# Optimization experiments

Measured on AMD Instinct MI355X. Metric: run time of the kernel, lower is better.

The kernel has to match this reference:

```python
import jax, jax.numpy as jnp
import numpy as np

B, C, H, W = 16, 256, 56, 56
WH, WW = 7, 7
NH = 8            # heads
HID = 1024        # mlp hidden = int(4*dim)
N = WH * WW
EPS = 1e-5


def _rel_index():
    # mirrors the torch buffer computation in Rel_Attention.__init__
    coords = np.stack(np.meshgrid(np.arange(WH), np.arange(WW), indexing='ij')).reshape(2, -1)  # (2, N)
    rel = coords[:, :, None] - coords[:, None, :]  # (2, N, N)
    rel[0] += WH - 1
    rel[1] += WW - 1
    rel[0] *= 2 * WW - 1
    return jnp.asarray(rel.sum(0).reshape(-1))  # (N*N,)

REL_IDX = _rel_index()


def channel_ln(x, w, b):
    # LayerNorm over channel dim of NCHW tensor (permute -> LN -> permute back)
    xt = x.transpose(0, 2, 3, 1)  # BHWC
    mu = xt.mean(-1, keepdims=True)
    var = xt.var(-1, keepdims=True)
    xt = (xt - mu) / jnp.sqrt(var + EPS) * w + b
    return xt.transpose(0, 3, 1, 2)


def to_blocks(x):
    # (B,C,H,W) -> (B, H/wh, W/ww, C, wh, ww)
    b, c, h, w = x.shape
    x = x.reshape(b, c, h // WH, WH, w // WW, WW)
    return x.transpose(0, 2, 4, 1, 3, 5)


def unblock(x):
    # faithful to original: reshape(B, C, Hb*win_W, Hb*win_W)  (square sizes)
    b, hb, wb, c, wh, ww = x.shape
    return x.transpose(0, 3, 1, 4, 2, 5).reshape(b, c, hb * ww, hb * ww)


def rel_attention(xw, qkv_w, qkv_b, proj_w, proj_b, table):
    b, hb, wb, c = xw.shape[:4]
    hd = c // NH
    scale = hd ** (-0.5)
    xf = xw.reshape(-1, c, N)                                  # (M, C, N)
    qkv = jnp.einsum('oc,mcn->mon', qkv_w, xf) + qkv_b[None, :, None]
    q, k, v = jnp.split(qkv, 3, axis=1)

    def heads(t):
        return t.reshape(-1, NH, hd, N).transpose(0, 1, 3, 2)  # (M, h, N, d)

    q, k, v = heads(q), heads(k), heads(v)
    bias = table[REL_IDX].reshape(N, N, NH).transpose(2, 0, 1)  # (h, N, N)
    attn = jnp.einsum('mhnd,mhkd->mhnk', q, k) * scale + bias
    attn = jax.nn.softmax(attn, axis=-1)
    o = jnp.einsum('mhnk,mhkd->mhnd', attn, v)                 # (M, h, N, d)
    o = o.transpose(0, 1, 3, 2).reshape(-1, c, N)              # (M, C, N)
    o = jnp.einsum('oc,mcn->mon', proj_w, o) + proj_b[None, :, None]
    return o.reshape(b, hb, wb, c, WH, WW)


def mlp(x, fc1_w, fc1_b, fc2_w, fc2_b):
    h = jnp.einsum('oc,bchw->bohw', fc1_w, x) + fc1_b[None, :, None, None]
    h = jax.nn.gelu(h, approximate=False)
    return jnp.einsum('oc,bchw->bohw', fc2_w, h) + fc2_b[None, :, None, None]


def setup_inputs() -> dict:
    key = jax.random.key(0)
    ks = jax.random.split(key, 8)
    s = 0.02
    return {
        'x': jax.random.normal(ks[0], (B, C, H, W), jnp.float32),
        'ln1_w': jnp.ones((C,), jnp.float32),
        'ln1_b': jnp.zeros((C,), jnp.float32),
        'ln2_w': jnp.ones((C,), jnp.float32),
        'ln2_b': jnp.zeros((C,), jnp.float32),
        'qkv_w': jax.random.normal(ks[1], (3 * C, C), jnp.float32) * s,
        'qkv_b': jnp.zeros((3 * C,), jnp.float32),
        'proj_w': jax.random.normal(ks[2], (C, C), jnp.float32) * s,
        'proj_b': jnp.zeros((C,), jnp.float32),
        'rel_bias_table': jax.random.normal(ks[3], ((2 * WH - 1) * (2 * WW - 1), NH), jnp.float32) * s,
        'fc1_w': jax.random.normal(ks[4], (HID, C), jnp.float32) * s,
        'fc1_b': jnp.zeros((HID,), jnp.float32),
        'fc2_w': jax.random.normal(ks[5], (C, HID), jnp.float32) * s,
        'fc2_b': jnp.zeros((C,), jnp.float32),
    }


def reference(x, ln1_w, ln1_b, ln2_w, ln2_b, qkv_w, qkv_b, proj_w, proj_b,
              rel_bias_table, fc1_w, fc1_b, fc2_w, fc2_b):
    out = to_blocks(channel_ln(x, ln1_w, ln1_b))
    out = rel_attention(out, qkv_w, qkv_b, proj_w, proj_b, rel_bias_table)
    # original applies attn a second time before unblocking
    out = rel_attention(out, qkv_w, qkv_b, proj_w, proj_b, rel_bias_table)
    x = x + unblock(out)
    x = x + mlp(channel_ln(x, ln2_w, ln2_b), fc1_w, fc1_b, fc2_w, fc2_b)
    return x
```

## Files before the change

kernel.cpp:

```cpp
#include <hip/hip_runtime.h>
#include <stdint.h>

typedef uint16_t u16;
typedef short bf16x8 __attribute__((ext_vector_type(8)));
typedef float f32x4 __attribute__((ext_vector_type(4)));

__device__ __forceinline__ float bf2f(u16 s) {
  union { unsigned int i; float f; } c; c.i = ((unsigned int)s) << 16; return c.f;
}
__device__ __forceinline__ u16 f2bf(float f) {
  union { float f; unsigned int i; } c; c.f = f;
  unsigned int u = c.i;
  u += 0x7FFFu + ((u >> 16) & 1u);
  return (u16)(u >> 16);
}
__device__ __forceinline__ f32x4 mfma16(bf16x8 a, bf16x8 b, f32x4 c) {
  return __builtin_amdgcn_mfma_f32_16x16x32_bf16(a, b, c, 0, 0, 0);
}
__device__ __forceinline__ int dtype_flag(const u16* ln1w_raw) { return ln1w_raw[0] == 0x3F80 ? 1 : 0; }
__device__ __forceinline__ float loadF(const void* p, size_t i, int flag) {
  return flag ? bf2f(((const u16*)p)[i]) : ((const float*)p)[i];
}

#define OFF_QKVW 0
#define OFF_QKVB 196608
#define OFF_PROJW 197376
#define OFF_PROJB 262912
#define OFF_REL 263168
#define OFF_FC1W 264520
#define OFF_FC1B 526664
#define OFF_FC2W 527688
#define OFF_FC2B 789832
#define OFF_LN1W 790088
#define OFF_LN1B 790344
#define OFF_LN2W 790600
#define OFF_LN2B 790856
#define WC_TOTAL 791112

__global__ __launch_bounds__(256) void k_convert(const u16* __restrict__ ln1w_raw,
    const void* qkvw, const void* qkvb, const void* projw, const void* projb,
    const void* rel, const void* fc1w, const void* fc1b, const void* fc2w, const void* fc2b,
    const void* ln1w, const void* ln1b, const void* ln2w, const void* ln2b,
    u16* __restrict__ dst) {
  const int flag = dtype_flag(ln1w_raw);
  int i = blockIdx.x * 256 + threadIdx.x;
  if (i >= WC_TOTAL) return;
  const void* src; int off;
  if      (i < OFF_QKVB)  { src = qkvw;  off = i - OFF_QKVW; }
  else if (i < OFF_PROJW) { src = qkvb;  off = i - OFF_QKVB; }
  else if (i < OFF_PROJB) { src = projw; off = i - OFF_PROJW; }
  else if (i < OFF_REL)   { src = projb; off = i - OFF_PROJB; }
  else if (i < OFF_FC1W)  { src = rel;   off = i - OFF_REL; }
  else if (i < OFF_FC1B)  { src = fc1w;  off = i - OFF_FC1W; }
  else if (i < OFF_FC2W)  { src = fc1b;  off = i - OFF_FC1B; }
  else if (i < OFF_FC2B)  { src = fc2w;  off = i - OFF_FC2W; }
  else if (i < OFF_LN1W)  { src = fc2b;  off = i - OFF_FC2B; }
  else if (i < OFF_LN1B)  { src = ln1w;  off = i - OFF_LN1W; }
  else if (i < OFF_LN2W)  { src = ln1b;  off = i - OFF_LN1B; }
  else if (i < OFF_LN2B)  { src = ln2w;  off = i - OFF_LN2W; }
  else                    { src = ln2b;  off = i - OFF_LN2B; }
  if (i < OFF_QKVB) {
    int j = off & 7, li = (off >> 3) & 63, c0i = (off >> 9) & 7, grp = off >> 12;
    off = (grp * 16 + (li & 15)) * 256 + c0i * 32 + (li >> 4) * 8 + j;
  } else if (i >= OFF_PROJW && i < OFF_PROJB) {
    int j = off & 7, li = (off >> 3) & 63, c0i = (off >> 9) & 7, grp = off >> 12;
    off = (grp * 16 + (li & 15)) * 256 + c0i * 32 + (li >> 4) * 8 + j;
  } else if (i >= OFF_FC1W && i < OFF_FC1B) {
    int j = off & 7, li = (off >> 3) & 63, hj = (off >> 9) & 1, c0i = (off >> 10) & 7,
        w = (off >> 13) & 3, ch = off >> 15;
    off = (ch * 128 + w * 32 + hj * 16 + (li & 15)) * 256 + c0i * 32 + (li >> 4) * 8 + j;
  } else if (i >= OFF_FC2W && i < OFF_FC2B) {
    int j = off & 7, li = (off >> 3) & 63, oct = (off >> 9) & 3, kki = (off >> 11) & 3,
        ch = (off >> 13) & 7, w = off >> 16;
    off = (w * 64 + oct * 16 + (li & 15)) * 1024 + ch * 128 + kki * 32 + (li >> 4) * 8 + j;
  }
  dst[i] = flag ? ((const u16*)src)[off] : f2bf(((const float*)src)[off]);
}

__global__ __launch_bounds__(256) void k_ln1b(const void* __restrict__ xin,
                                              const u16* __restrict__ ln1w_raw,
                                              const u16* __restrict__ lw,
                                              const u16* __restrict__ lb,
                                              u16* __restrict__ win) {
  const int flag = dtype_flag(ln1w_raw);
  __shared__ float tile[56 * 257];
  __shared__ float smu[56], srs[56];
  const int bid = blockIdx.x;
  const int b = bid / 56, h = bid - b * 56;
  const int t = threadIdx.x;
  const int hb = h / 7, ph = h - hb * 7;
  {
    const int lane = t & 63, wq = t >> 6;
    if (lane < 56) {
#pragma unroll 4
      for (int ci = 0; ci < 64; ++ci) {
        const int c = ci * 4 + wq;
        const size_t addr = ((size_t)(b * 256 + c) * 56 + h) * 56 + lane;
        tile[lane * 257 + c] = loadF(xin, addr, flag);
      }
    }
  }
  __syncthreads();
  {
    const int row = t >> 2, qq = t & 3;
    float s = 0.f, q = 0.f;
    if (row < 56) {
      const float* tr = &tile[row * 257 + qq];
#pragma unroll 8
      for (int c0 = 0; c0 < 64; ++c0) { float v = tr[c0 * 4]; s += v; q += v * v; }
    }
    s += __shfl_xor(s, 1, 64); q += __shfl_xor(q, 1, 64);
    s += __shfl_xor(s, 2, 64); q += __shfl_xor(q, 2, 64);
    if (row < 56 && qq == 0) {
      float mm = s * (1.f / 256.f);
      float var = q * (1.f / 256.f) - mm * mm;
      smu[row] = mm; srs[row] = rsqrtf(var + 1e-5f);
    }
  }
  __syncthreads();
#pragma unroll
  for (int i = 0; i < 7; ++i) {
    int eid8 = i * 256 + t;
    int wp = eid8 >> 5, c8 = (eid8 & 31) << 3;
    const float mm = smu[wp], rs = srs[wp];
    const int m = b * 64 + hb * 8 + (wp / 7), n = ph * 7 + (wp % 7);
    bf16x8 o;
#pragma unroll
    for (int j = 0; j < 8; ++j) {
      int c = c8 + j;
      o[j] = (short)f2bf((tile[wp * 257 + c] - mm) * rs * bf2f(lw[c]) + bf2f(lb[c]));
    }
    *(bf16x8*)&win[(size_t)m * 12544 + n * 256 + c8] = o;
  }
}

__global__ __launch_bounds__(512) void k_attn_stage(const u16* __restrict__ win,
                                                    const u16* __restrict__ qkvw,
                                                    const u16* __restrict__ qkvb,
                                                    const u16* __restrict__ rel,
                                                    const u16* __restrict__ projw,
                                                    const u16* __restrict__ projb,
                                                    u16* __restrict__ wout) {
  __shared__ __align__(16) u16 xs[64 * 264];
  __shared__ __align__(16) u16 wa[8][7424];
  const int m = blockIdx.x;
  const int t = threadIdx.x;
  const int w = t >> 6, li = t & 63, lane = li & 15, quad = li >> 4;
  const int hg = w;
  const f32x4 z = {0.f, 0.f, 0.f, 0.f};
  const u16* src = win + (size_t)m * 12544;
#pragma unroll
  for (int i = 0; i < 4; ++i) {
    int chunk = i * 512 + t;
    if (chunk < 1568) {
      int n = chunk >> 5, cc = (chunk & 31) << 3;
      *(bf16x8*)&xs[n * 264 + cc] = *(const bf16x8*)&src[chunk << 3];
    }
  }
  for (int i = t; i < 15 * 264; i += 512) xs[49 * 264 + i] = 0;
  u16* qw = wa[w];
  u16* kw = wa[w] + 2560;
  u16* vw = wa[w] + 5120;
  u16* Pw = wa[w];
  u16* Os = xs;
  for (int i = li; i < 15 * 40; i += 64) { qw[49 * 40 + i] = 0; kw[49 * 40 + i] = 0; }
  for (int i = li; i < 32 * 15; i += 64) { int d = i / 15, j = i - d * 15; vw[d * 72 + 49 + j] = 0; }
  __syncthreads();
  const float SCALE = 0.17677669529663687f;
#pragma unroll
  for (int part = 0; part < 2; ++part) {
    const int obase = part * 256 + hg * 32;
    f32x4 acc[4][2];
#pragma unroll
    for (int i = 0; i < 4; ++i) { acc[i][0] = z; acc[i][1] = z; }
#pragma unroll
    for (int c0i = 0; c0i < 8; ++c0i) {
      bf16x8 a[4], b[2];
#pragma unroll
      for (int nt = 0; nt < 4; ++nt)
        a[nt] = *(const bf16x8*)&xs[(nt * 16 + lane) * 264 + c0i * 32 + quad * 8];
#pragma unroll
      for (int oj = 0; oj < 2; ++oj)
        b[oj] = *(const bf16x8*)&qkvw[(size_t)(((part * 16 + hg * 2 + oj) * 8 + c0i) * 64 + li) * 8];
#pragma unroll
      for (int nt = 0; nt < 4; ++nt)
#pragma unroll
        for (int oj = 0; oj < 2; ++oj) acc[nt][oj] = mfma16(a[nt], b[oj], acc[nt][oj]);
    }
    u16* dstL = part ? kw : qw;
#pragma unroll
    for (int oj = 0; oj < 2; ++oj) {
      const int d = oj * 16 + lane;
      const float bias = bf2f(qkvb[obase + d]);
#pragma unroll
      for (int nt = 0; nt < 4; ++nt)
#pragma unroll
        for (int r = 0; r < 4; ++r) {
          int n = nt * 16 + quad * 4 + r;
          if (n < 49) dstL[n * 40 + d] = f2bf(acc[nt][oj][r] + bias);
        }
    }
  }
  {
    f32x4 acc[2][4];
#pragma unroll
    for (int i = 0; i < 2; ++i)
#pragma unroll
      for (int j = 0; j < 4; ++j) acc[i][j] = z;
#pragma unroll
    for (int c0i = 0; c0i < 8; ++c0i) {
      bf16x8 a[2], b[4];
#pragma unroll
      for (int vj = 0; vj < 2; ++vj)
        a[vj] = *(const bf16x8*)&qkvw[(size_t)(((32 + hg * 2 + vj) * 8 + c0i) * 64 + li) * 8];
#pragma unroll
      for (int nt = 0; nt < 4; ++nt)
        b[nt] = *(const bf16x8*)&xs[(nt * 16 + lane) * 264 + c0i * 32 + quad * 8];
#pragma unroll
      for (int vj = 0; vj < 2; ++vj)
#pragma unroll
        for (int nt = 0; nt < 4; ++nt) acc[vj][nt] = mfma16(a[vj], b[nt], acc[vj][nt]);
    }
#pragma unroll
    for (int vj = 0; vj < 2; ++vj)
#pragma unroll
      for (int r = 0; r < 4; ++r) {
        const int d = vj * 16 + quad * 4 + r;
        const float bias = bf2f(qkvb[512 + hg * 32 + d]);
#pragma unroll
        for (int nt = 0; nt < 4; ++nt) {
          int n = nt * 16 + lane;
          if (n < 49) vw[d * 72 + n] = f2bf(acc[vj][nt][r] + bias);
        }
      }
  }
  __syncthreads();
  f32x4 s[4][4];
  {
    bf16x8 aq[4], bk[4];
#pragma unroll
    for (int nt = 0; nt < 4; ++nt) {
      aq[nt] = *(const bf16x8*)&qw[(nt * 16 + lane) * 40 + quad * 8];
      bk[nt] = *(const bf16x8*)&kw[(nt * 16 + lane) * 40 + quad * 8];
    }
#pragma unroll
    for (int i = 0; i < 4; ++i)
#pragma unroll
      for (int j = 0; j < 4; ++j) s[i][j] = mfma16(aq[i], bk[j], z);
  }
#pragma unroll
  for (int nt1 = 0; nt1 < 4; ++nt1) {
#pragma unroll
    for (int r = 0; r < 4; ++r) {
      int n1 = nt1 * 16 + quad * 4 + r;
      int n1c = n1 < 49 ? n1 : 48;
      int ph1 = n1c / 7, pw1 = n1c - ph1 * 7;
      float v[4];
#pragma unroll
      for (int j = 0; j < 4; ++j) {
        int n2 = j * 16 + lane;
        if (n2 < 49) {
          int ph2 = n2 / 7, pw2 = n2 - ph2 * 7;
          int idx = (ph1 - ph2 + 6) * 13 + (pw1 - pw2 + 6);
          v[j] = s[nt1][j][r] * SCALE + bf2f(rel[idx * 8 + hg]);
        } else v[j] = -1e30f;
      }
      float mx = fmaxf(fmaxf(v[0], v[1]), fmaxf(v[2], v[3]));
      for (int off = 1; off < 16; off <<= 1) mx = fmaxf(mx, __shfl_xor(mx, off, 64));
      float e0 = __expf(v[0] - mx), e1 = __expf(v[1] - mx);
      float e2 = __expf(v[2] - mx), e3 = __expf(v[3] - mx);
      float sum = e0 + e1 + e2 + e3;
      for (int off = 1; off < 16; off <<= 1) sum += __shfl_xor(sum, off, 64);
      float rinv = __builtin_amdgcn_rcpf(sum);
      Pw[n1 * 72 + 0 * 16 + lane] = f2bf(e0 * rinv);
      Pw[n1 * 72 + 1 * 16 + lane] = f2bf(e1 * rinv);
      Pw[n1 * 72 + 2 * 16 + lane] = f2bf(e2 * rinv);
      Pw[n1 * 72 + 3 * 16 + lane] = f2bf(e3 * rinv);
    }
  }
  {
    f32x4 o[4][2];
#pragma unroll
    for (int i = 0; i < 4; ++i) { o[i][0] = z; o[i][1] = z; }
#pragma unroll
    for (int kc = 0; kc < 2; ++kc) {
      bf16x8 ap[4], bv[2];
#pragma unroll
      for (int nt1 = 0; nt1 < 4; ++nt1)
        ap[nt1] = *(const bf16x8*)&Pw[(nt1 * 16 + lane) * 72 + kc * 32 + quad * 8];
#pragma unroll
      for (int dt = 0; dt < 2; ++dt)
        bv[dt] = *(const bf16x8*)&vw[(dt * 16 + lane) * 72 + kc * 32 + quad * 8];
#pragma unroll
      for (int nt1 = 0; nt1 < 4; ++nt1)
#pragma unroll
        for (int dt = 0; dt < 2; ++dt) o[nt1][dt] = mfma16(ap[nt1], bv[dt], o[nt1][dt]);
    }
#pragma unroll
    for (int nt1 = 0; nt1 < 4; ++nt1)
#pragma unroll
      for (int dt = 0; dt < 2; ++dt)
#pragma unroll
        for (int r = 0; r < 4; ++r) {
          int n1 = nt1 * 16 + quad * 4 + r;
          if (n1 < 49) Os[n1 * 264 + hg * 32 + dt * 16 + lane] = f2bf(o[nt1][dt][r]);
        }
  }
  __syncthreads();
  {
    f32x4 acc[4][2];
#pragma unroll
    for (int i = 0; i < 4; ++i) { acc[i][0] = z; acc[i][1] = z; }
#pragma unroll
    for (int c0i = 0; c0i < 8; ++c0i) {
      bf16x8 a[4], b[2];
#pragma unroll
      for (int nt = 0; nt < 4; ++nt)
        a[nt] = *(const bf16x8*)&Os[(nt * 16 + lane) * 264 + c0i * 32 + quad * 8];
#pragma unroll
      for (int oj = 0; oj < 2; ++oj)
        b[oj] = *(const bf16x8*)&projw[(size_t)(((w * 2 + oj) * 8 + c0i) * 64 + li) * 8];
#pragma unroll
      for (int nt = 0; nt < 4; ++nt)
#pragma unroll
        for (int oj = 0; oj < 2; ++oj) acc[nt][oj] = mfma16(a[nt], b[oj], acc[nt][oj]);
    }
#pragma unroll
    for (int oj = 0; oj < 2; ++oj) {
      const int oc = w * 32 + oj * 16 + lane;
      const float bias = bf2f(projb[oc]);
#pragma unroll
      for (int nt = 0; nt < 4; ++nt)
#pragma unroll
        for (int r = 0; r < 4; ++r) {
          int n = nt * 16 + quad * 4 + r;
          if (n < 49) wout[(size_t)m * 12544 + n * 256 + oc] = f2bf(acc[nt][oj][r] + bias);
        }
    }
  }
}

__global__ __launch_bounds__(256) void k_resid2(const void* __restrict__ xin,
                                                const u16* __restrict__ ln1w_raw,
                                                const u16* __restrict__ attn,
                                                const u16* __restrict__ l2w,
                                                const u16* __restrict__ l2b,
                                                u16* __restrict__ xrn,
                                                u16* __restrict__ ln2d) {
  const int flag = dtype_flag(ln1w_raw);
  __shared__ float tile[56 * 257];
  __shared__ float smu[56], srs[56];
  const int bid = blockIdx.x;
  const int b = bid / 56, h = bid - b * 56;
  const int t = threadIdx.x;
  const int hb = h / 7, ph = h - hb * 7;
#pragma unroll
  for (int i = 0; i < 7; ++i) {
    int eid8 = i * 256 + t;
    int wp = eid8 >> 5, c8 = (eid8 & 31) << 3;
    int mm = b * 64 + hb * 8 + (wp / 7), nn = ph * 7 + (wp % 7);
    bf16x8 v = *(const bf16x8*)&attn[(size_t)mm * 12544 + nn * 256 + c8];
    float* dst = &tile[wp * 257 + c8];
#pragma unroll
    for (int j = 0; j < 8; ++j) dst[j] = bf2f((u16)v[j]);
  }
  __syncthreads();
  {
    const int lane = t & 63, wq = t >> 6;
    if (lane < 56) {
#pragma unroll 4
      for (int ci = 0; ci < 64; ++ci) {
        const int c = ci * 4 + wq;
        const size_t addr = ((size_t)(b * 256 + c) * 56 + h) * 56 + lane;
        float v = tile[lane * 257 + c] + loadF(xin, addr, flag);
        tile[lane * 257 + c] = v;
        xrn[addr] = f2bf(v);
      }
    }
  }
  __syncthreads();
  {
    const int row = t >> 2, qq = t & 3;
    float s = 0.f, q = 0.f;
    if (row < 56) {
      const float* tr = &tile[row * 257 + qq];
#pragma unroll 8
      for (int c0 = 0; c0 < 64; ++c0) { float v = tr[c0 * 4]; s += v; q += v * v; }
    }
    s += __shfl_xor(s, 1, 64); q += __shfl_xor(q, 1, 64);
    s += __shfl_xor(s, 2, 64); q += __shfl_xor(q, 2, 64);
    if (row < 56 && qq == 0) {
      float mm = s * (1.f / 256.f);
      float var = q * (1.f / 256.f) - mm * mm;
      smu[row] = mm; srs[row] = rsqrtf(var + 1e-5f);
    }
  }
  __syncthreads();
#pragma unroll
  for (int i = 0; i < 7; ++i) {
    int eid8 = i * 256 + t;
    int wp = eid8 >> 5, c8 = (eid8 & 31) << 3;
    const float mm = smu[wp], rs = srs[wp];
    bf16x8 o;
#pragma unroll
    for (int j = 0; j < 8; ++j) {
      int c = c8 + j;
      o[j] = (short)f2bf((tile[wp * 257 + c] - mm) * rs * bf2f(l2w[c]) + bf2f(l2b[c]));
    }
    const int p = b * 3136 + h * 56 + wp;
    const int pblk = p >> 6, pt = (p & 63) >> 4, r16 = p & 15;
    const int c0i = c8 >> 5, quad = (c8 >> 3) & 3;
    *(bf16x8*)&ln2d[(size_t)((((pblk * 4 + pt) * 8 + c0i) * 64 + quad * 16 + r16)) << 3] = o;
  }
}

__global__ __launch_bounds__(256, 3) void k_mlp2(const u16* __restrict__ aG,
                                                 const u16* __restrict__ w1,
                                                 const u16* __restrict__ b1,
                                                 const u16* __restrict__ w2,
                                                 const u16* __restrict__ b2,
                                                 const u16* __restrict__ xrn,
                                                 const u16* __restrict__ ln1w_raw,
                                                 void* __restrict__ out) {
  const int flag = dtype_flag(ln1w_raw);
  __shared__ __align__(16) u16 arena[25088];
  u16* xp = arena;
  u16* g  = arena + 16384;
  const int pblk = blockIdx.x;
  const int pix0 = pblk * 64;
  const int t = threadIdx.x;
  const int w = t >> 6, li = t & 63, lane = li & 15, quad = li >> 4;
  {
    const u16* asrc = aG + (size_t)pblk * 16384;
#pragma unroll
    for (int i = 0; i < 8; ++i) {
      int idx = i * 256 + t;
      *(bf16x8*)&xp[idx * 8] = *(const bf16x8*)&asrc[(size_t)idx * 8];
    }
  }
  __syncthreads();
  const f32x4 z = {0.f, 0.f, 0.f, 0.f};
  f32x4 acc2[4][4];
#pragma unroll
  for (int i = 0; i < 4; ++i)
#pragma unroll
    for (int j = 0; j < 4; ++j) acc2[i][j] = z;

  auto fc1 = [&](int ch) {
    f32x4 a1[4][2];
#pragma unroll
    for (int i = 0; i < 4; ++i) { a1[i][0] = z; a1[i][1] = z; }
#pragma unroll
    for (int c0i = 0; c0i < 8; ++c0i) {
      bf16x8 av[4], bw[2];
#pragma unroll
      for (int pt = 0; pt < 4; ++pt)
        av[pt] = *(const bf16x8*)&xp[((pt * 8 + c0i) * 64 + li) * 8];
#pragma unroll
      for (int hj = 0; hj < 2; ++hj)
        bw[hj] = *(const bf16x8*)&w1[(size_t)((((ch * 4 + w) * 8 + c0i) * 2 + hj) * 64 + li) * 8];
#pragma unroll
      for (int pt = 0; pt < 4; ++pt)
#pragma unroll
        for (int hj = 0; hj < 2; ++hj) a1[pt][hj] = mfma16(av[pt], bw[hj], a1[pt][hj]);
    }
#pragma unroll
    for (int hj = 0; hj < 2; ++hj) {
      const int hl = w * 32 + hj * 16 + lane;
      const float bias = bf2f(b1[ch * 128 + hl]);
#pragma unroll
      for (int pt = 0; pt < 4; ++pt)
#pragma unroll
        for (int r = 0; r < 4; ++r) {
          float u_ = a1[pt][hj][r] + bias;
          float y = u_ * fmaf(u_ * u_, 0.035677408136300125f, 0.7978845608028654f);
          float e2 = __expf(-2.f * y);
          float v = u_ * __builtin_amdgcn_rcpf(1.f + e2);
          g[(pt * 16 + quad * 4 + r) * 136 + hl] = f2bf(v);
        }
    }
  };
  auto fc2 = [&](int ch) {
#pragma unroll
    for (int kki = 0; kki < 4; ++kki) {
      bf16x8 aw[4], bg[4];
#pragma unroll
      for (int oct = 0; oct < 4; ++oct)
        aw[oct] = *(const bf16x8*)&w2[(size_t)((((w * 8 + ch) * 4 + kki) * 4 + oct) * 64 + li) * 8];
#pragma unroll
      for (int pt = 0; pt < 4; ++pt)
        bg[pt] = *(const bf16x8*)&g[(pt * 16 + lane) * 136 + kki * 32 + quad * 8];
#pragma unroll
      for (int oct = 0; oct < 4; ++oct)
#pragma unroll
        for (int pt = 0; pt < 4; ++pt) acc2[oct][pt] = mfma16(aw[oct], bg[pt], acc2[oct][pt]);
    }
  };

  fc1(0);
  __syncthreads();
#pragma unroll 1
  for (int ch = 0; ch < 8; ++ch) {
    fc2(ch);
    if (ch < 7) {
      __syncthreads();
      fc1(ch + 1);
      __syncthreads();
    }
  }

  float* Ob = (float*)arena;
  const int b_ = pix0 / 3136, rem0 = pix0 - b_ * 3136;
  const int sub = t & 7, r0 = t >> 3;
#pragma unroll 1
  for (int e = 0; e < 2; ++e) {
    __syncthreads();
    if ((w >> 1) == e) {
      const int wl = w & 1;
#pragma unroll
      for (int oct = 0; oct < 4; ++oct)
#pragma unroll
        for (int pt = 0; pt < 4; ++pt)
#pragma unroll
          for (int r = 0; r < 4; ++r)
            Ob[(wl * 64 + oct * 16 + quad * 4 + r) * 65 + pt * 16 + lane] = acc2[oct][pt][r];
    }
    __syncthreads();
    bf16x8 xr[4];
    size_t addrs[4];
#pragma unroll
    for (int i = 0; i < 4; ++i) {
      const int oc = e * 128 + i * 32 + r0;
      addrs[i] = (size_t)(b_ * 256 + oc) * 3136 + rem0 + sub * 8;
      xr[i] = *(const bf16x8*)&xrn[addrs[i]];
    }
#pragma unroll
    for (int i = 0; i < 4; ++i) {
      const int oc = e * 128 + i * 32 + r0;
      const float bias = bf2f(b2[oc]);
      const float* obr = &Ob[(i * 32 + r0) * 65 + sub * 8];
      float v[8];
#pragma unroll
      for (int j = 0; j < 8; ++j)
        v[j] = obr[j] + bias + bf2f((u16)xr[i][j]);
      if (flag) {
        bf16x8 o8;
#pragma unroll
        for (int j = 0; j < 8; ++j) o8[j] = (short)f2bf(v[j]);
        *(bf16x8*)&((u16*)out)[addrs[i]] = o8;
      } else {
        float* dst = &((float*)out)[addrs[i]];
        f32x4 lo = {v[0], v[1], v[2], v[3]}, hi = {v[4], v[5], v[6], v[7]};
        *(f32x4*)&dst[0] = lo;
        *(f32x4*)&dst[4] = hi;
      }
    }
  }
}

extern "C" void kernel_launch(void* const* d_in, const int* in_sizes, int n_in,
                              void* d_out, int out_size, void* d_ws, size_t ws_size,
                              hipStream_t stream) {
  (void)in_sizes; (void)n_in; (void)out_size; (void)ws_size;
  const void* x     = d_in[0];
  const u16* ln1w_raw = (const u16*)d_in[1];
  u16* ws = (u16*)d_ws;
  const size_t R = 12845056;
  u16* R0 = ws;
  u16* R1 = ws + R;
  u16* R2 = ws + 2 * R;
  u16* WC = ws + 3 * R;
  const u16* qkvw_c = WC + OFF_QKVW;
  const u16* qkvb_c = WC + OFF_QKVB;
  const u16* projw_c = WC + OFF_PROJW;
  const u16* projb_c = WC + OFF_PROJB;
  const u16* rel_c  = WC + OFF_REL;
  const u16* fc1w_c = WC + OFF_FC1W;
  const u16* fc1b_c = WC + OFF_FC1B;
  const u16* fc2w_c = WC + OFF_FC2W;
  const u16* fc2b_c = WC + OFF_FC2B;
  const u16* ln1w_c = WC + OFF_LN1W;
  const u16* ln1b_c = WC + OFF_LN1B;
  const u16* ln2w_c = WC + OFF_LN2W;
  const u16* ln2b_c = WC + OFF_LN2B;

  k_convert<<<(WC_TOTAL + 255) / 256, 256, 0, stream>>>(
      ln1w_raw, d_in[5], d_in[6], d_in[7], d_in[8], d_in[9],
      d_in[10], d_in[11], d_in[12], d_in[13], d_in[1], d_in[2], d_in[3], d_in[4], WC);

  k_ln1b      <<<896, 256, 0, stream>>>(x, ln1w_raw, ln1w_c, ln1b_c, R0);
  k_attn_stage<<<1024, 512, 0, stream>>>(R0, qkvw_c, qkvb_c, rel_c, projw_c, projb_c, R1);
  k_attn_stage<<<1024, 512, 0, stream>>>(R1, qkvw_c, qkvb_c, rel_c, projw_c, projb_c, R2);
  k_resid2    <<<896, 256, 0, stream>>>(x, ln1w_raw, R2, ln2w_c, ln2b_c, R0, R1);
  k_mlp2      <<<784, 256, 0, stream>>>(R1, fc1w_c, fc1b_c, fc2w_c, fc2b_c, R0, ln1w_raw, d_out);
}
```

Before: 515.5 us.

## Fuse both attention passes into one kernel and vectorize LN global loads

The two back-to-back attention stage launches become one kernel that loops twice over the same window. The first pass's projection output is written back into the shared-memory input tile instead of global memory, which removes one launch and a full global write and read of the intermediate. The LN1 and residual kernels now load x with 16-byte vector loads along W and store the residual as packed vectors. MFMA sections are wrapped in s_setprio raises. In exchange there are extra barriers and longer-lived blocks, and register pressure may rise.

After: 792.1 us. +53.7%, slower.

```diff
diff --git a/kernel.cpp b/kernel.cpp
--- a/kernel.cpp
+++ b/kernel.cpp
@@ -2,6 +2,7 @@
 #include <stdint.h>
 
 typedef uint16_t u16;
+typedef short bf16x4 __attribute__((ext_vector_type(4)));
 typedef short bf16x8 __attribute__((ext_vector_type(8)));
 typedef float f32x4 __attribute__((ext_vector_type(4)));
 
@@ -89,15 +90,25 @@
   const int b = bid / 56, h = bid - b * 56;
   const int t = threadIdx.x;
   const int hb = h / 7, ph = h - hb * 7;
-  {
-    const int lane = t & 63, wq = t >> 6;
-    if (lane < 56) {
-#pragma unroll 4
-      for (int ci = 0; ci < 64; ++ci) {
-        const int c = ci * 4 + wq;
-        const size_t addr = ((size_t)(b * 256 + c) * 56 + h) * 56 + lane;
-        tile[lane * 257 + c] = loadF(xin, addr, flag);
-      }
+  if (!flag) {
+#pragma unroll
+    for (int i = 0; i < 14; ++i) {
+      int chunk = i * 256 + t;
+      int c = chunk / 14, w4 = (chunk - c * 14) * 4;
+      const float* xp4 = (const float*)xin + ((size_t)(b * 256 + c) * 56 + h) * 56 + w4;
+      f32x4 v = *(const f32x4*)xp4;
+#pragma unroll
+      for (int k = 0; k < 4; ++k) tile[(w4 + k) * 257 + c] = v[k];
+    }
+  } else {
+#pragma unroll
+    for (int i = 0; i < 7; ++i) {
+      int chunk = i * 256 + t;
+      int c = chunk / 7, w8 = (chunk - c * 7) * 8;
+      const u16* xp8 = (const u16*)xin + ((size_t)(b * 256 + c) * 56 + h) * 56 + w8;
+      bf16x8 v = *(const bf16x8*)xp8;
+#pragma unroll
+      for (int k = 0; k < 8; ++k) tile[(w8 + k) * 257 + c] = bf2f((u16)v[k]);
     }
   }
   __syncthreads();
@@ -167,175 +178,205 @@
   for (int i = li; i < 32 * 15; i += 64) { int d = i / 15, j = i - d * 15; vw[d * 72 + 49 + j] = 0; }
   __syncthreads();
   const float SCALE = 0.17677669529663687f;
-#pragma unroll
-  for (int part = 0; part < 2; ++part) {
-    const int obase = part * 256 + hg * 32;
-    f32x4 acc[4][2];
-#pragma unroll
-    for (int i = 0; i < 4; ++i) { acc[i][0] = z; acc[i][1] = z; }
-#pragma unroll
-    for (int c0i = 0; c0i < 8; ++c0i) {
-      bf16x8 a[4], b[2];
-#pragma unroll
-      for (int nt = 0; nt < 4; ++nt)
-        a[nt] = *(const bf16x8*)&xs[(nt * 16 + lane) * 264 + c0i * 32 + quad * 8];
-#pragma unroll
-      for (int oj = 0; oj < 2; ++oj)
-        b[oj] = *(const bf16x8*)&qkvw[(size_t)(((part * 16 + hg * 2 + oj) * 8 + c0i) * 64 + li) * 8];
-#pragma unroll
-      for (int nt = 0; nt < 4; ++nt)
-#pragma unroll
-        for (int oj = 0; oj < 2; ++oj) acc[nt][oj] = mfma16(a[nt], b[oj], acc[nt][oj]);
-    }
-    u16* dstL = part ? kw : qw;
-#pragma unroll
-    for (int oj = 0; oj < 2; ++oj) {
-      const int d = oj * 16 + lane;
-      const float bias = bf2f(qkvb[obase + d]);
-#pragma unroll
-      for (int nt = 0; nt < 4; ++nt)
+#pragma unroll 1
+  for (int s_ = 0; s_ < 2; ++s_) {
+#pragma unroll
+    for (int part = 0; part < 2; ++part) {
+      const int obase = part * 256 + hg * 32;
+      f32x4 acc[4][2];
+#pragma unroll
+      for (int i = 0; i < 4; ++i) { acc[i][0] = z; acc[i][1] = z; }
+#pragma unroll
+      for (int c0i = 0; c0i < 8; ++c0i) {
+        bf16x8 a[4], b[2];
+#pragma unroll
+        for (int nt = 0; nt < 4; ++nt)
+          a[nt] = *(const bf16x8*)&xs[(nt * 16 + lane) * 264 + c0i * 32 + quad * 8];
+#pragma unroll
+        for (int oj = 0; oj < 2; ++oj)
+          b[oj] = *(const bf16x8*)&qkvw[(size_t)(((part * 16 + hg * 2 + oj) * 8 + c0i) * 64 + li) * 8];
+        __builtin_amdgcn_s_setprio(1);
+#pragma unroll
+        for (int nt = 0; nt < 4; ++nt)
+#pragma unroll
+          for (int oj = 0; oj < 2; ++oj) acc[nt][oj] = mfma16(a[nt], b[oj], acc[nt][oj]);
+        __builtin_amdgcn_s_setprio(0);
+      }
+      u16* dstL = part ? kw : qw;
+#pragma unroll
+      for (int oj = 0; oj < 2; ++oj) {
+        const int d = oj * 16 + lane;
+        const float bias = bf2f(qkvb[obase + d]);
+#pragma unroll
+        for (int nt = 0; nt < 4; ++nt)
+#pragma unroll
+          for (int r = 0; r < 4; ++r) {
+            int n = nt * 16 + quad * 4 + r;
+            if (n < 49) dstL[n * 40 + d] = f2bf(acc[nt][oj][r] + bias);
+          }
+      }
+    }
+    {
+      f32x4 acc[2][4];
+#pragma unroll
+      for (int i = 0; i < 2; ++i)
+#pragma unroll
+        for (int j = 0; j < 4; ++j) acc[i][j] = z;
+#pragma unroll
+      for (int c0i = 0; c0i < 8; ++c0i) {
+        bf16x8 a[2], b[4];
+#pragma unroll
+        for (int vj = 0; vj < 2; ++vj)
+          a[vj] = *(const bf16x8*)&qkvw[(size_t)(((32 + hg * 2 + vj) * 8 + c0i) * 64 + li) * 8];
+#pragma unroll
+        for (int nt = 0; nt < 4; ++nt)
+          b[nt] = *(const bf16x8*)&xs[(nt * 16 + lane) * 264 + c0i * 32 + quad * 8];
+        __builtin_amdgcn_s_setprio(1);
+#pragma unroll
+        for (int vj = 0; vj < 2; ++vj)
+#pragma unroll
+          for (int nt = 0; nt < 4; ++nt) acc[vj][nt] = mfma16(a[vj], b[nt], acc[vj][nt]);
+        __builtin_amdgcn_s_setprio(0);
+      }
+#pragma unroll
+      for (int vj = 0; vj < 2; ++vj)
 #pragma unroll
         for (int r = 0; r < 4; ++r) {
-          int n = nt * 16 + quad * 4 + r;
-          if (n < 49) dstL[n * 40 + d] = f2bf(acc[nt][oj][r] + bias);
+          const int d = vj * 16 + quad * 4 + r;
+          const float bias = bf2f(qkvb[512 + hg * 32 + d]);
+#pragma unroll
+          for (int nt = 0; nt < 4; ++nt) {
+            int n = nt * 16 + lane;
+            if (n < 49) vw[d * 72 + n] = f2bf(acc[vj][nt][r] + bias);
+          }
         }
     }
-  }
-  {
-    f32x4 acc[2][4];
-#pragma unroll
-    for (int i = 0; i < 2; ++i)
-#pragma unroll
-      for (int j = 0; j < 4; ++j) acc[i][j] = z;
-#pragma unroll
-    for (int c0i = 0; c0i < 8; ++c0i) {
-      bf16x8 a[2], b[4];
-#pragma unroll
-      for (int vj = 0; vj < 2; ++vj)
-        a[vj] = *(const bf16x8*)&qkvw[(size_t)(((32 + hg * 2 + vj) * 8 + c0i) * 64 + li) * 8];
-#pragma unroll
-      for (int nt = 0; nt < 4; ++nt)
-        b[nt] = *(const bf16x8*)&xs[(nt * 16 + lane) * 264 + c0i * 32 + quad * 8];
-#pragma unroll
-      for (int vj = 0; vj < 2; ++vj)
-#pragma unroll
-        for (int nt = 0; nt < 4; ++nt) acc[vj][nt] = mfma16(a[vj], b[nt], acc[vj][nt]);
-    }
-#pragma unroll
-    for (int vj = 0; vj < 2; ++vj)
+    __syncthreads();
+    f32x4 s[4][4];
+    {
+      bf16x8 aq[4], bk[4];
+#pragma unroll
+      for (int nt = 0; nt < 4; ++nt) {
+        aq[nt] = *(const bf16x8*)&qw[(nt * 16 + lane) * 40 + quad * 8];
+        bk[nt] = *(const bf16x8*)&kw[(nt * 16 + lane) * 40 + quad * 8];
+      }
+      __builtin_amdgcn_s_setprio(1);
+#pragma unroll
+      for (int i = 0; i < 4; ++i)
+#pragma unroll
+        for (int j = 0; j < 4; ++j) s[i][j] = mfma16(aq[i], bk[j], z);
+      __builtin_amdgcn_s_setprio(0);
+    }
+#pragma unroll
+    for (int nt1 = 0; nt1 < 4; ++nt1) {
 #pragma unroll
       for (int r = 0; r < 4; ++r) {
-        const int d = vj * 16 + quad * 4 + r;
-        const float bias = bf2f(qkvb[512 + hg * 32 + d]);
-#pragma unroll
-        for (int nt = 0; nt < 4; ++nt) {
-          int n = nt * 16 + lane;
-          if (n < 49) vw[d * 72 + n] = f2bf(acc[vj][nt][r] + bias);
+        int n1 = nt1 * 16 + quad * 4 + r;
+        int n1c = n1 < 49 ? n1 : 48;
+        int ph1 = n1c / 7, pw1 = n1c - ph1 * 7;
+        float v[4];
+#pragma unroll
+        for (int j = 0; j < 4; ++j) {
+          int n2 = j * 16 + lane;
+          if (n2 < 49) {
+            int ph2 = n2 / 7, pw2 = n2 - ph2 * 7;
+            int idx = (ph1 - ph2 + 6) * 13 + (pw1 - pw2 + 6);
+            v[j] = s[nt1][j][r] * SCALE + bf2f(rel[idx * 8 + hg]);
+          } else v[j] = -1e30f;
         }
-      }
-  }
-  __syncthreads();
-  f32x4 s[4][4];
-  {
-    bf16x8 aq[4], bk[4];
-#pragma unroll
-    for (int nt = 0; nt < 4; ++nt) {
-      aq[nt] = *(const bf16x8*)&qw[(nt * 16 + lane) * 40 + quad * 8];
-      bk[nt] = *(const bf16x8*)&kw[(nt * 16 + lane) * 40 + quad * 8];
-    }
-#pragma unroll
-    for (int i = 0; i < 4; ++i)
-#pragma unroll
-      for (int j = 0; j < 4; ++j) s[i][j] = mfma16(aq[i], bk[j], z);
-  }
-#pragma unroll
-  for (int nt1 = 0; nt1 < 4; ++nt1) {
-#pragma unroll
-    for (int r = 0; r < 4; ++r) {
-      int n1 = nt1 * 16 + quad * 4 + r;
-      int n1c = n1 < 49 ? n1 : 48;
-      int ph1 = n1c / 7, pw1 = n1c - ph1 * 7;
-      float v[4];
-#pragma unroll
-      for (int j = 0; j < 4; ++j) {
-        int n2 = j * 16 + lane;
-        if (n2 < 49) {
-          int ph2 = n2 / 7, pw2 = n2 - ph2 * 7;
-          int idx = (ph1 - ph2 + 6) * 13 + (pw1 - pw2 + 6);
-          v[j] = s[nt1][j][r] * SCALE + bf2f(rel[idx * 8 + hg]);
-        } else v[j] = -1e30f;
-      }
-      float mx = fmaxf(fmaxf(v[0], v[1]), fmaxf(v[2], v[3]));
-      for (int off = 1; off < 16; off <<= 1) mx = fmaxf(mx, __shfl_xor(mx, off, 64));
-      float e0 = __expf(v[0] - mx), e1 = __expf(v[1] - mx);
-      float e2 = __expf(v[2] - mx), e3 = __expf(v[3] - mx);
-      float sum = e0 + e1 + e2 + e3;
-      for (int off = 1; off < 16; off <<= 1) sum += __shfl_xor(sum, off, 64);
-      float rinv = __builtin_amdgcn_rcpf(sum);
-      Pw[n1 * 72 + 0 * 16 + lane] = f2bf(e0 * rinv);
-      Pw[n1 * 72 + 1 * 16 + lane] = f2bf(e1 * rinv);
-      Pw[n1 * 72 + 2 * 16 + lane] = f2bf(e2 * rinv);
-      Pw[n1 * 72 + 3 * 16 + lane] = f2bf(e3 * rinv);
-    }
-  }
-  {
-    f32x4 o[4][2];
-#pragma unroll
-    for (int i = 0; i < 4; ++i) { o[i][0] = z; o[i][1] = z; }
-#pragma unroll
-    for (int kc = 0; kc < 2; ++kc) {
-      bf16x8 ap[4], bv[2];
+        float mx = fmaxf(fmaxf(v[0], v[1]), fmaxf(v[2], v[3]));
+        for (int off = 1; off < 16; off <<= 1) mx = fmaxf(mx, __shfl_xor(mx, off, 64));
+        float e0 = __expf(v[0] - mx), e1 = __expf(v[1] - mx);
+        float e2 = __expf(v[2] - mx), e3 = __expf(v[3] - mx);
+        float sum = e0 + e1 + e2 + e3;
+        for (int off = 1; off < 16; off <<= 1) sum += __shfl_xor(sum, off, 64);
+        float rinv = __builtin_amdgcn_rcpf(sum);
+        Pw[n1 * 72 + 0 * 16 + lane] = f2bf(e0 * rinv);
+        Pw[n1 * 72 + 1 * 16 + lane] = f2bf(e1 * rinv);
+        Pw[n1 * 72 + 2 * 16 + lane] = f2bf(e2 * rinv);
+        Pw[n1 * 72 + 3 * 16 + lane] = f2bf(e3 * rinv);
+      }
+    }
+    {
+      f32x4 o[4][2];
+#pragma unroll
+      for (int i = 0; i < 4; ++i) { o[i][0] = z; o[i][1] = z; }
+#pragma unroll
+      for (int kc = 0; kc < 2; ++kc) {
+        bf16x8 ap[4], bv[2];
+#pragma unroll
+        for (int nt1 = 0; nt1 < 4; ++nt1)
+          ap[nt1] = *(const bf16x8*)&Pw[(nt1 * 16 + lane) * 72 + kc * 32 + quad * 8];
+#pragma unroll
+        for (int dt = 0; dt < 2; ++dt)
+          bv[dt] = *(const bf16x8*)&vw[(dt * 16 + lane) * 72 + kc * 32 + quad * 8];
+        __builtin_amdgcn_s_setprio(1);
+#pragma unroll
+        for (int nt1 = 0; nt1 < 4; ++nt1)
+#pragma unroll
+          for (int dt = 0; dt < 2; ++dt) o[nt1][dt] = mfma16(ap[nt1], bv[dt], o[nt1][dt]);
+        __builtin_amdgcn_s_setprio(0);
+      }
 #pragma unroll
       for (int nt1 = 0; nt1 < 4; ++nt1)
-        ap[nt1] = *(const bf16x8*)&Pw[(nt1 * 16 + lane) * 72 + kc * 32 + quad * 8];
-#pragma unroll
-      for (int dt = 0; dt < 2; ++dt)
-        bv[dt] = *(const bf16x8*)&vw[(dt * 16 + lane) * 72 + kc * 32 + quad * 8];
-#pragma unroll
-      for (int nt1 = 0; nt1 < 4; ++nt1)
-#pragma unroll
-        for (int dt = 0; dt < 2; ++dt) o[nt1][dt] = mfma16(ap[nt1], bv[dt], o[nt1][dt]);
-    }
-#pragma unroll
-    for (int nt1 = 0; nt1 < 4; ++nt1)
-#pragma unroll
-      for (int dt = 0; dt < 2; ++dt)
-#pragma unroll
-        for (int r = 0; r < 4; ++r) {
-          int n1 = nt1 * 16 + quad * 4 + r;
-          if (n1 < 49) Os[n1 * 264 + hg * 32 + dt * 16 + lane] = f2bf(o[nt1][dt][r]);
+#pragma unroll
+        for (int dt = 0; dt < 2; ++dt)
+#pragma unroll
+          for (int r = 0; r < 4; ++r) {
+            int n1 = nt1 * 16 + quad * 4 + r;
+            if (n1 < 49) Os[n1 * 264 + hg * 32 + dt * 16 + lane] = f2bf(o[nt1][dt][r]);
+          }
+    }
+    __syncthreads();
+    {
+      f32x4 acc[4][2];
+#pragma unroll
+      for (int i = 0; i < 4; ++i) { acc[i][0] = z; acc[i][1] = z; }
+#pragma unroll
+      for (int c0i = 0; c0i < 8; ++c0i) {
+        bf16x8 a[4], b[2];
+#pragma unroll
+        for (int nt = 0; nt < 4; ++nt)
+          a[nt] = *(const bf16x8*)&Os[(nt * 16 + lane) * 264 + c0i * 32 + quad * 8];
+#pragma unroll
+        for (int oj = 0; oj < 2; ++oj)
+          b[oj] = *(const bf16x8*)&projw[(size_t)(((w * 2 + oj) * 8 + c0i) * 64 + li) * 8];
+        __builtin_amdgcn_s_setprio(1);
+#pragma unroll
+        for (int nt = 0; nt < 4; ++nt)
+#pragma unroll
+          for (int oj = 0; oj < 2; ++oj) acc[nt][oj] = mfma16(a[nt], b[oj], acc[nt][oj]);
+        __builtin_amdgcn_s_setprio(0);
+      }
+      __syncthreads();
+      if (s_ == 0) {
+#pragma unroll
+        for (int oj = 0; oj < 2; ++oj) {
+          const int oc = w * 32 + oj * 16 + lane;
+          const float bias = bf2f(projb[oc]);
+#pragma unroll
+          for (int nt = 0; nt < 4; ++nt)
+#pragma unroll
+            for (int r = 0; r < 4; ++r) {
+              int n = nt * 16 + quad * 4 + r;
+              if (n < 49) xs[n * 264 + oc] = f2bf(acc[nt][oj][r] + bias);
+            }
         }
-  }
-  __syncthreads();
-  {
-    f32x4 acc[4][2];
-#pragma unroll
-    for (int i = 0; i < 4; ++i) { acc[i][0] = z; acc[i][1] = z; }
-#pragma unroll
-    for (int c0i = 0; c0i < 8; ++c0i) {
-      bf16x8 a[4], b[2];
-#pragma unroll
-      for (int nt = 0; nt < 4; ++nt)
-        a[nt] = *(const bf16x8*)&Os[(nt * 16 + lane) * 264 + c0i * 32 + quad * 8];
-#pragma unroll
-      for (int oj = 0; oj < 2; ++oj)
-        b[oj] = *(const bf16x8*)&projw[(size_t)(((w * 2 + oj) * 8 + c0i) * 64 + li) * 8];
-#pragma unroll
-      for (int nt = 0; nt < 4; ++nt)
-#pragma unroll
-        for (int oj = 0; oj < 2; ++oj) acc[nt][oj] = mfma16(a[nt], b[oj], acc[nt][oj]);
-    }
-#pragma unroll
-    for (int oj = 0; oj < 2; ++oj) {
-      const int oc = w * 32 + oj * 16 + lane;
-      const float bias = bf2f(projb[oc]);
-#pragma unroll
-      for (int nt = 0; nt < 4; ++nt)
-#pragma unroll
-        for (int r = 0; r < 4; ++r) {
-          int n = nt * 16 + quad * 4 + r;
-          if (n < 49) wout[(size_t)m * 12544 + n * 256 + oc] = f2bf(acc[nt][oj][r] + bias);
+        __syncthreads();
+      } else {
+#pragma unroll
+        for (int oj = 0; oj < 2; ++oj) {
+          const int oc = w * 32 + oj * 16 + lane;
+          const float bias = bf2f(projb[oc]);
+#pragma unroll
+          for (int nt = 0; nt < 4; ++nt)
+#pragma unroll
+            for (int r = 0; r < 4; ++r) {
+              int n = nt * 16 + quad * 4 + r;
+              if (n < 49) wout[(size_t)m * 12544 + n * 256 + oc] = f2bf(acc[nt][oj][r] + bias);
+            }
         }
+      }
     }
   }
 }
@@ -365,17 +406,37 @@
     for (int j = 0; j < 8; ++j) dst[j] = bf2f((u16)v[j]);
   }
   __syncthreads();
-  {
-    const int lane = t & 63, wq = t >> 6;
-    if (lane < 56) {
-#pragma unroll 4
-      for (int ci = 0; ci < 64; ++ci) {
-        const int c = ci * 4 + wq;
-        const size_t addr = ((size_t)(b * 256 + c) * 56 + h) * 56 + lane;
-        float v = tile[lane * 257 + c] + loadF(xin, addr, flag);
-        tile[lane * 257 + c] = v;
-        xrn[addr] = f2bf(v);
-      }
+  if (!flag) {
+#pragma unroll
+    for (int i = 0; i < 14; ++i) {
+      int chunk = i * 256 + t;
+      int c = chunk / 14, w4 = (chunk - c * 14) * 4;
+      const size_t base = ((size_t)(b * 256 + c) * 56 + h) * 56 + w4;
+      f32x4 xv = *(const f32x4*)((const float*)xin + base);
+      bf16x4 o4;
+#pragma unroll
+      for (int k = 0; k < 4; ++k) {
+        float v = tile[(w4 + k) * 257 + c] + xv[k];
+        tile[(w4 + k) * 257 + c] = v;
+        o4[k] = (short)f2bf(v);
+      }
+      *(bf16x4*)&xrn[base] = o4;
+    }
+  } else {
+#pragma unroll
+    for (int i = 0; i < 7; ++i) {
+      int chunk = i * 256 + t;
+      int c = chunk / 7, w8 = (chunk - c * 7) * 8;
+      const size_t base = ((size_t)(b * 256 + c) * 56 + h) * 56 + w8;
+      bf16x8 xv = *(const bf16x8*)((const u16*)xin + base);
+      bf16x8 o8;
+#pragma unroll
+      for (int k = 0; k < 8; ++k) {
+        float v = tile[(w8 + k) * 257 + c] + bf2f((u16)xv[k]);
+        tile[(w8 + k) * 257 + c] = v;
+        o8[k] = (short)f2bf(v);
+      }
+      *(bf16x8*)&xrn[base] = o8;
     }
   }
   __syncthreads();
@@ -589,8 +650,7 @@
       d_in[10], d_in[11], d_in[12], d_in[13], d_in[1], d_in[2], d_in[3], d_in[4], WC);
 
   k_ln1b      <<<896, 256, 0, stream>>>(x, ln1w_raw, ln1w_c, ln1b_c, R0);
-  k_attn_stage<<<1024, 512, 0, stream>>>(R0, qkvw_c, qkvb_c, rel_c, projw_c, projb_c, R1);
-  k_attn_stage<<<1024, 512, 0, stream>>>(R1, qkvw_c, qkvb_c, rel_c, projw_c, projb_c, R2);
+  k_attn_stage<<<1024, 512, 0, stream>>>(R0, qkvw_c, qkvb_c, rel_c, projw_c, projb_c, R2);
   k_resid2    <<<896, 256, 0, stream>>>(x, ln1w_raw, R2, ln2w_c, ln2b_c, R0, R1);
   k_mlp2      <<<784, 256, 0, stream>>>(R1, fc1w_c, fc1b_c, fc2w_c, fc2b_c, R0, ln1w_raw, d_out);
 }
```
